# Performance work log

Hardware: AMD Instinct MI355X
Metric: run time of the kernel (lower is better)

## Reference

```python
import jax, jax.numpy as jnp
import numpy as np

LN_EPS = 1e-5

def layer_norm(h, gamma, beta):
    mu = jnp.mean(h, axis=-1, keepdims=True)
    var = jnp.mean(jnp.square(h - mu), axis=-1, keepdims=True)
    return (h - mu) * jax.lax.rsqrt(var + LN_EPS) * gamma + beta

def gcn_conv(x, src, dst, W, b, n_nodes):
    # PyG GCNConv: h = X W; out = D^-1/2 (A + I) D^-1/2 h + b
    h = x @ W
    deg = jax.ops.segment_sum(jnp.ones_like(src, dtype=h.dtype), dst, num_segments=n_nodes)
    dinv = jax.lax.rsqrt(jnp.maximum(deg, 1.0))  # deg >= 1 due to self-loops
    norm = dinv[src] * dinv[dst]                  # [E]
    msg = h[src] * norm[:, None]                  # [E, d]
    return jax.ops.segment_sum(msg, dst, num_segments=n_nodes) + b

def setup_inputs() -> dict:
    key = jax.random.key(0)
    ks = jax.random.split(key, 8)
    N, E, Cin, Ch, Cout = 10000, 160000, 256, 512, 256
    x = jax.random.normal(ks[0], (N, Cin), dtype=jnp.float32)
    edge_index = jax.random.randint(ks[1], (2, E), 0, N, dtype=jnp.int64)
    W1 = jax.random.normal(ks[2], (Cin, Ch), dtype=jnp.float32) * (1.0 / np.sqrt(Cin))
    b1 = jnp.zeros((Ch,), dtype=jnp.float32)
    gamma1 = jnp.ones((Ch,), dtype=jnp.float32)
    beta1 = jnp.zeros((Ch,), dtype=jnp.float32)
    W2 = jax.random.normal(ks[3], (Ch, Cout), dtype=jnp.float32) * (1.0 / np.sqrt(Ch))
    b2 = jnp.zeros((Cout,), dtype=jnp.float32)
    gamma2 = jnp.ones((Cout,), dtype=jnp.float32)
    beta2 = jnp.zeros((Cout,), dtype=jnp.float32)
    return {"x": x, "edge_index": edge_index, "W1": W1, "b1": b1,
            "gamma1": gamma1, "beta1": beta1, "W2": W2, "b2": b2,
            "gamma2": gamma2, "beta2": beta2}

def reference(x, edge_index, W1, b1, gamma1, beta1, W2, b2, gamma2, beta2):
    n = x.shape[0]
    loops = jnp.arange(n, dtype=edge_index.dtype)
    src = jnp.concatenate([edge_index[0], loops])
    dst = jnp.concatenate([edge_index[1], loops])
    h = gcn_conv(x, src, dst, W1, b1, n)
    h = jax.nn.relu(layer_norm(h, gamma1, beta1))  # dropout = identity (eval mode)
    g = gcn_conv(h, src, dst, W2, b2, n)
    g = jax.nn.relu(layer_norm(g, gamma2, beta2))
    return g
```

## Files before the change

### kernel.cpp

```cpp
#include <hip/hip_runtime.h>
#include <hip/hip_bf16.h>


typedef __attribute__((ext_vector_type(8))) short bf16x8;
typedef __attribute__((ext_vector_type(4))) float f32x4;
typedef __attribute__((ext_vector_type(4))) unsigned short us4;
typedef __attribute__((ext_vector_type(8))) unsigned short us8;

__device__ __forceinline__ unsigned short f2bf(float f) {
  unsigned int x = __float_as_uint(f);
  return (unsigned short)((x + 0x7FFFu + ((x >> 16) & 1u)) >> 16);
}
__device__ __forceinline__ float bf2f(unsigned short u) {
  return __uint_as_float((unsigned int)u << 16);
}

__device__ __forceinline__ void transpose_tile(const float* __restrict__ W,
                                               unsigned short* __restrict__ Wt,
                                               int K, int N, int n0, int k0,
                                               unsigned short (*t)[33], int tid) {
  int tx = tid & 31, ty = tid >> 5;
#pragma unroll
  for (int i = 0; i < 32; i += 8)
    t[ty + i][tx] = f2bf(W[(size_t)(k0 + ty + i) * N + n0 + tx]);
  __syncthreads();
#pragma unroll
  for (int i = 0; i < 32; i += 8)
    Wt[(size_t)(n0 + ty + i) * K + k0 + tx] = t[tx][ty + i];
  __syncthreads();
}

__global__ __launch_bounds__(256) void prep_kernel(
    const float* __restrict__ x, unsigned short* __restrict__ xb, long nelem,
    const int* __restrict__ dst, int E, int* __restrict__ deg,
    const float* __restrict__ W1, unsigned short* __restrict__ W1t,
    const float* __restrict__ W2, unsigned short* __restrict__ W2t,
    int Cin, int Ch, int Cout, int nbx, int nbe, int nbw1) {
  __shared__ unsigned short t[32][33];
  int bid = blockIdx.x, tid = threadIdx.x;
  if (bid < nbx) {
    long i = ((long)bid * 256 + tid) * 8;
    if (i + 8 <= nelem) {
      f32x4 a = *(const f32x4*)&x[i];
      f32x4 b = *(const f32x4*)&x[i + 4];
      us8 o;
      o[0] = f2bf(a.x); o[1] = f2bf(a.y); o[2] = f2bf(a.z); o[3] = f2bf(a.w);
      o[4] = f2bf(b.x); o[5] = f2bf(b.y); o[6] = f2bf(b.z); o[7] = f2bf(b.w);
      *(us8*)&xb[i] = o;
    }
  } else if (bid < nbx + nbe) {
    int e = (bid - nbx) * 256 + tid;
    if (e < E) atomicAdd(&deg[dst[e]], 1);
  } else if (bid < nbx + nbe + nbw1) {
    int ti = bid - nbx - nbe;
    int w = Ch >> 5;
    transpose_tile(W1, W1t, Cin, Ch, (ti % w) * 32, (ti / w) * 32, t, tid);
  } else {
    int ti = bid - nbx - nbe - nbw1;
    int w = Cout >> 5;
    transpose_tile(W2, W2t, Ch, Cout, (ti % w) * 32, (ti / w) * 32, t, tid);
  }
}

__global__ __launch_bounds__(1024) void scan_kernel(const int* __restrict__ deg, int N,
                                                    int* __restrict__ offsets,
                                                    int* __restrict__ curs,
                                                    float* __restrict__ dinv) {
  __shared__ int wsum[16];
  __shared__ int chunk_base;
  int tid = threadIdx.x;
  int lane = tid & 63, wid = tid >> 6;
  if (tid == 0) chunk_base = 0;
  __syncthreads();
  for (int c = 0; c < N; c += 1024) {
    int i = c + tid;
    int v = (i < N) ? deg[i] : 0;
    if (i < N) dinv[i] = rsqrtf((float)(v + 1));
    int s = v;
#pragma unroll
    for (int off = 1; off < 64; off <<= 1) {
      int t = __shfl_up(s, off, 64);
      if (lane >= off) s += t;
    }
    if (lane == 63) wsum[wid] = s;
    __syncthreads();
    if (wid == 0 && lane < 16) {
      int ws = wsum[lane];
      int t = ws;
#pragma unroll
      for (int off = 1; off < 16; off <<= 1) {
        int u = __shfl_up(t, off, 64);
        if (lane >= off) t += u;
      }
      wsum[lane] = t - ws;
    }
    __syncthreads();
    if (i < N) {
      int o = chunk_base + wsum[wid] + s - v;
      offsets[i] = o;
      curs[i] = o;
    }
    __syncthreads();
    if (tid == 1023) chunk_base += wsum[15] + s;
  }
  __syncthreads();
  if (tid == 0) offsets[N] = chunk_base;
}

__global__ __launch_bounds__(256) void fill_kernel(const int* __restrict__ src,
                                                   const int* __restrict__ dst, int E,
                                                   int* __restrict__ curs,
                                                   const float* __restrict__ dinv,
                                                   int2* __restrict__ csr_sn) {
  int e = blockIdx.x * 256 + threadIdx.x;
  if (e >= E) return;
  int s = src[e], d = dst[e];
  int p = atomicAdd(&curs[d], 1);
  csr_sn[p] = make_int2(s, __float_as_int(dinv[s] * dinv[d]));
}


#define AGG_FMA(hv, wt)                      \
  acc.x = fmaf(bf2f((hv).x), (wt), acc.x);   \
  acc.y = fmaf(bf2f((hv).y), (wt), acc.y);   \
  acc.z = fmaf(bf2f((hv).z), (wt), acc.z);   \
  acc.w = fmaf(bf2f((hv).w), (wt), acc.w);

template <bool FUSE_LN, typename OutT>
__device__ __forceinline__ void agg_node(int node, int lane,
                                         const unsigned short* __restrict__ H,
                                         const int2* __restrict__ csr,
                                         const int* __restrict__ offs,
                                         const float* __restrict__ dinv,
                                         const float* __restrict__ bias,
                                         const float* __restrict__ gamma,
                                         const float* __restrict__ beta,
                                         OutT* __restrict__ out) {
  int p0 = offs[node], p1 = offs[node + 1];
  int n = p1 - p0;
  f32x4 acc = {0.f, 0.f, 0.f, 0.f};
  if (n > 0) {
    int2 e0 = csr[p0];
    us4 h0 = *(const us4*)&H[(size_t)e0.x * 256 + lane * 4];
    if (n > 1) {
      int2 e1 = csr[p0 + 1];
      for (int p = p0; p + 2 < p1; ++p) {
        us4 h1v = *(const us4*)&H[(size_t)e1.x * 256 + lane * 4];
        int2 e2 = csr[p + 2];
        AGG_FMA(h0, __int_as_float(e0.y));
        e0 = e1; h0 = h1v; e1 = e2;
      }
      us4 h1v = *(const us4*)&H[(size_t)e1.x * 256 + lane * 4];
      AGG_FMA(h0, __int_as_float(e0.y));
      AGG_FMA(h1v, __int_as_float(e1.y));
    } else {
      AGG_FMA(h0, __int_as_float(e0.y));
    }
  }
  float dn = dinv[node];
  us4 sv = *(const us4*)&H[(size_t)node * 256 + lane * 4];
  AGG_FMA(sv, dn * dn);
  if (bias) acc += *(const f32x4*)&bias[lane * 4];
  if constexpr (FUSE_LN) {
    float s  = acc.x + acc.y + acc.z + acc.w;
    float ss = acc.x * acc.x + acc.y * acc.y + acc.z * acc.z + acc.w * acc.w;
#pragma unroll
    for (int off = 32; off > 0; off >>= 1) {
      s  += __shfl_xor(s, off, 64);
      ss += __shfl_xor(ss, off, 64);
    }
    float mu = s * (1.0f / 256.0f);
    float var = ss * (1.0f / 256.0f) - mu * mu;
    float r = rsqrtf(var + 1e-5f);
    f32x4 g  = *(const f32x4*)&gamma[lane * 4];
    f32x4 be = *(const f32x4*)&beta[lane * 4];
    f32x4 o;
    o.x = fmaxf((acc.x - mu) * r * g.x + be.x, 0.f);
    o.y = fmaxf((acc.y - mu) * r * g.y + be.y, 0.f);
    o.z = fmaxf((acc.z - mu) * r * g.z + be.z, 0.f);
    o.w = fmaxf((acc.w - mu) * r * g.w + be.w, 0.f);
    *(f32x4*)&out[(size_t)node * 256 + lane * 4] = o;
  } else {
    us4 o;
    o.x = f2bf(acc.x); o.y = f2bf(acc.y); o.z = f2bf(acc.z); o.w = f2bf(acc.w);
    *(us4*)&out[(size_t)node * 256 + lane * 4] = o;
  }
}

template <bool FUSE_LN, typename OutT>
__global__ __launch_bounds__(256) void agg_kernel(const unsigned short* __restrict__ H,
                                                  const int2* __restrict__ csr,
                                                  const int* __restrict__ offs,
                                                  const float* __restrict__ dinv,
                                                  const float* __restrict__ bias,
                                                  const float* __restrict__ gamma,
                                                  const float* __restrict__ beta,
                                                  OutT* __restrict__ out, int N) {
  int node = blockIdx.x * 4 + (threadIdx.x >> 6);
  if (node >= N) return;
  agg_node<FUSE_LN, OutT>(node, threadIdx.x & 63, H, csr, offs, dinv, bias, gamma, beta, out);
}


template <typename OutT>
__global__ __launch_bounds__(256) void mfma_gemm_kernel(
    const unsigned short* __restrict__ A, const unsigned short* __restrict__ Bt,
    const float* __restrict__ bias, OutT* __restrict__ C, int M, int K, int N) {
  __shared__ unsigned short As[2][64 * 32];
  __shared__ unsigned short Bs[2][128 * 32];
  int tid = threadIdx.x;
  int lane = tid & 63, wid = tid >> 6;
  int bm = blockIdx.x * 64, bn = blockIdx.y * 128;
  int wm = (wid >> 1) * 32, wn = (wid & 1) * 64;
  int srow = tid >> 2;
  int schunk = tid & 3;
  int frow = lane & 15, fk = lane >> 4;
  f32x4 acc[2][4] = {};

  int scA = schunk ^ ((srow >> 1) & 3);
  int gaA = bm + srow; gaA = gaA < M ? gaA : M - 1;
  const unsigned short* gA0 = A + (size_t)gaA * K + scA * 8;
  int rowB0 = srow, rowB1 = 64 + srow;
  int scB0 = schunk ^ ((rowB0 >> 1) & 3);
  int scB1 = schunk ^ ((rowB1 >> 1) & 3);
  const unsigned short* gB0 = Bt + (size_t)(bn + rowB0) * K + scB0 * 8;
  const unsigned short* gB1 = Bt + (size_t)(bn + rowB1) * K + scB1 * 8;

  auto stage = [&](int k0, unsigned short* Ad, unsigned short* Bd) {
    __builtin_amdgcn_global_load_lds(
        (const __attribute__((address_space(1))) unsigned int*)(const void*)(gA0 + k0),
        (__attribute__((address_space(3))) unsigned int*)(void*)(Ad + (wid * 16) * 32),
        16, 0, 0);
    __builtin_amdgcn_global_load_lds(
        (const __attribute__((address_space(1))) unsigned int*)(const void*)(gB0 + k0),
        (__attribute__((address_space(3))) unsigned int*)(void*)(Bd + (wid * 16) * 32),
        16, 0, 0);
    __builtin_amdgcn_global_load_lds(
        (const __attribute__((address_space(1))) unsigned int*)(const void*)(gB1 + k0),
        (__attribute__((address_space(3))) unsigned int*)(void*)(Bd + (64 + wid * 16) * 32),
        16, 0, 0);
  };

  int nk = K >> 5;
  stage(0, As[0], Bs[0]);
  __syncthreads();
  for (int k = 0; k < nk; ++k) {
    unsigned short* Ac = As[k & 1];
    unsigned short* Bc = Bs[k & 1];
    if (k + 1 < nk) stage((k + 1) << 5, As[(k + 1) & 1], Bs[(k + 1) & 1]);
    bf16x8 af[2], bf[4];
#pragma unroll
    for (int mi = 0; mi < 2; ++mi) {
      int row = wm + mi * 16 + frow;
      int sc = fk ^ ((row >> 1) & 3);
      af[mi] = *(const bf16x8*)(Ac + row * 32 + sc * 8);
    }
#pragma unroll
    for (int ni = 0; ni < 4; ++ni) {
      int row = wn + ni * 16 + frow;
      int sc = fk ^ ((row >> 1) & 3);
      bf[ni] = *(const bf16x8*)(Bc + row * 32 + sc * 8);
    }
#pragma unroll
    for (int mi = 0; mi < 2; ++mi)
#pragma unroll
      for (int ni = 0; ni < 4; ++ni)
        acc[mi][ni] = __builtin_amdgcn_mfma_f32_16x16x32_bf16(af[mi], bf[ni], acc[mi][ni], 0, 0, 0);
    __syncthreads();
  }

  int row0 = bm + wm + fk * 4;
  int col0 = bn + wn + frow;
#pragma unroll
  for (int mi = 0; mi < 2; ++mi) {
#pragma unroll
    for (int ni = 0; ni < 4; ++ni) {
      int col = col0 + ni * 16;
      float bv = bias ? bias[col] : 0.0f;
#pragma unroll
      for (int r = 0; r < 4; ++r) {
        int row = row0 + mi * 16 + r;
        if (row < M) {
          float v = acc[mi][ni][r] + bv;
          if constexpr (sizeof(OutT) == 4) C[(size_t)row * N + col] = v;
          else                             C[(size_t)row * N + col] = f2bf(v);
        }
      }
    }
  }
}


__global__ __launch_bounds__(256) void ln_relu512_kernel(const float* __restrict__ in,
                                                         const float* __restrict__ gamma,
                                                         const float* __restrict__ beta,
                                                         unsigned short* __restrict__ out) {
  int row = blockIdx.x;
  const float* p = in + (size_t)row * 512;
  int tid = threadIdx.x;
  float v0 = p[tid];
  float v1 = p[tid + 256];
  float s = v0 + v1;
  float ss = v0 * v0 + v1 * v1;
#pragma unroll
  for (int off = 32; off > 0; off >>= 1) {
    s  += __shfl_down(s, off, 64);
    ss += __shfl_down(ss, off, 64);
  }
  __shared__ float sh[8];
  int wid = tid >> 6;
  if ((tid & 63) == 0) { sh[wid] = s; sh[4 + wid] = ss; }
  __syncthreads();
  s  = sh[0] + sh[1] + sh[2] + sh[3];
  ss = sh[4] + sh[5] + sh[6] + sh[7];
  float mu = s * (1.0f / 512.0f);
  float var = ss * (1.0f / 512.0f) - mu * mu;
  float r = rsqrtf(var + 1e-5f);
  out[(size_t)row * 512 + tid]       = f2bf(fmaxf((v0 - mu) * r * gamma[tid] + beta[tid], 0.0f));
  out[(size_t)row * 512 + tid + 256] = f2bf(fmaxf((v1 - mu) * r * gamma[tid + 256] + beta[tid + 256], 0.0f));
}


extern "C" void kernel_launch(void* const* d_in, const int* in_sizes, int n_in,
                              void* d_out, int out_size, void* d_ws, size_t ws_size,
                              hipStream_t stream) {
  const float* x    = (const float*)d_in[0];
  const int*   ei   = (const int*)d_in[1];
  const float* W1   = (const float*)d_in[2];
  const float* b1   = (const float*)d_in[3];
  const float* ga1  = (const float*)d_in[4];
  const float* be1  = (const float*)d_in[5];
  const float* W2   = (const float*)d_in[6];
  const float* b2   = (const float*)d_in[7];
  const float* ga2  = (const float*)d_in[8];
  const float* be2  = (const float*)d_in[9];
  float* out = (float*)d_out;

  const int Ch   = in_sizes[3];
  const int Cout = in_sizes[7];
  const int Cin  = in_sizes[2] / Ch;
  const int N    = in_sizes[0] / Cin;
  const int E    = in_sizes[1] / 2;
  const int* srcp = ei;
  const int* dstp = ei + E;

  char* ws = (char*)d_ws;
  size_t off = 0;
  auto alloc = [&](size_t bytes) -> void* {
    off = (off + 255) & ~(size_t)255;
    void* p = ws + off;
    off += bytes;
    return p;
  };
  unsigned short* xb   = (unsigned short*)alloc((size_t)N * Cin * 2);
  unsigned short* axb  = (unsigned short*)alloc((size_t)N * Cin * 2);
  float*          h1   = (float*)alloc((size_t)N * Ch * 4);
  unsigned short* h1b  = (unsigned short*)alloc((size_t)N * Ch * 2);
  unsigned short* h2b  = (unsigned short*)alloc((size_t)N * Cout * 2);
  unsigned short* W1t  = (unsigned short*)alloc((size_t)Cin * Ch * 2);
  unsigned short* W2t  = (unsigned short*)alloc((size_t)Ch * Cout * 2);
  int*   deg   = (int*)alloc((size_t)N * 4);
  int*   curs  = (int*)alloc((size_t)N * 4);
  int*   offs  = (int*)alloc((size_t)(N + 1) * 4);
  float* dinv  = (float*)alloc((size_t)N * 4);
  int2*  csr   = (int2*)alloc((size_t)E * 8);

  hipMemsetAsync(deg, 0, (size_t)N * 4, stream);

  long nelem = (long)N * Cin;
  int nbx  = (int)((nelem / 8 + 255) / 256);
  int nbe  = (E + 255) / 256;
  int nbw1 = (Cin / 32) * (Ch / 32);
  int nbw2 = (Ch / 32) * (Cout / 32);
  prep_kernel<<<nbx + nbe + nbw1 + nbw2, 256, 0, stream>>>(
      x, xb, nelem, dstp, E, deg, W1, W1t, W2, W2t, Cin, Ch, Cout, nbx, nbe, nbw1);
  scan_kernel<<<1, 1024, 0, stream>>>(deg, N, offs, curs, dinv);
  fill_kernel<<<nbe, 256, 0, stream>>>(srcp, dstp, E, curs, dinv, csr);

  agg_kernel<false, unsigned short><<<(N + 3) / 4, 256, 0, stream>>>(
      xb, csr, offs, dinv, nullptr, nullptr, nullptr, axb, N);
  mfma_gemm_kernel<float><<<dim3((N + 63) / 64, Ch / 128), 256, 0, stream>>>(
      axb, W1t, b1, h1, N, Cin, Ch);
  ln_relu512_kernel<<<N, 256, 0, stream>>>(h1, ga1, be1, h1b);

  mfma_gemm_kernel<unsigned short><<<dim3((N + 63) / 64, Cout / 128), 256, 0, stream>>>(
      h1b, W2t, nullptr, h2b, N, Ch, Cout);
  agg_kernel<true, float><<<(N + 3) / 4, 256, 0, stream>>>(
      h2b, csr, offs, dinv, b2, ga2, be2, out, N);
}
```

Measured before the change: 189.9 us.

## Reorder layer-1 GCN to GEMM-then-aggregate and fuse LayerNorm into aggregation

Layer 1 now multiplies X by W1 first, then aggregates the 512-wide bf16 result with bias, LayerNorm and ReLU fused into the aggregation kernel. The aggregation kernel is generalised over channel width. This removes the fp32 intermediate and the standalone LayerNorm kernel. In exchange, the sparse gather in layer 1 reads rows twice as wide, and the GEMM output is rounded to bf16 before aggregation.

```diff
diff --git a/kernel.cpp b/kernel.cpp
--- a/kernel.cpp
+++ b/kernel.cpp
@@ -6,6 +6,10 @@
 typedef __attribute__((ext_vector_type(4))) float f32x4;
 typedef __attribute__((ext_vector_type(4))) unsigned short us4;
 typedef __attribute__((ext_vector_type(8))) unsigned short us8;
+
+template <int CW> struct VecT;
+template <> struct VecT<4> { typedef us4 T; };
+template <> struct VecT<8> { typedef us8 T; };
 
 __device__ __forceinline__ unsigned short f2bf(float f) {
   unsigned int x = __float_as_uint(f);
@@ -120,92 +124,77 @@
 }
 
 
-#define AGG_FMA(hv, wt)                      \
-  acc.x = fmaf(bf2f((hv).x), (wt), acc.x);   \
-  acc.y = fmaf(bf2f((hv).y), (wt), acc.y);   \
-  acc.z = fmaf(bf2f((hv).z), (wt), acc.z);   \
-  acc.w = fmaf(bf2f((hv).w), (wt), acc.w);
-
-template <bool FUSE_LN, typename OutT>
-__device__ __forceinline__ void agg_node(int node, int lane,
-                                         const unsigned short* __restrict__ H,
-                                         const int2* __restrict__ csr,
-                                         const int* __restrict__ offs,
-                                         const float* __restrict__ dinv,
-                                         const float* __restrict__ bias,
-                                         const float* __restrict__ gamma,
-                                         const float* __restrict__ beta,
-                                         OutT* __restrict__ out) {
+template <int C, typename OutT>
+__global__ __launch_bounds__(256) void agg_ln_kernel(
+    const unsigned short* __restrict__ H, const int2* __restrict__ csr,
+    const int* __restrict__ offs, const float* __restrict__ dinv,
+    const float* __restrict__ bias, const float* __restrict__ gamma,
+    const float* __restrict__ beta, OutT* __restrict__ out, int N) {
+  constexpr int CW = C / 64;
+  typedef typename VecT<CW>::T usv;
+  int node = blockIdx.x * 4 + (threadIdx.x >> 6);
+  if (node >= N) return;
+  int lane = threadIdx.x & 63;
   int p0 = offs[node], p1 = offs[node + 1];
   int n = p1 - p0;
-  f32x4 acc = {0.f, 0.f, 0.f, 0.f};
+  float acc[CW] = {};
+  auto fma_row = [&](usv hv, float wt) {
+#pragma unroll
+    for (int j = 0; j < CW; ++j) acc[j] = fmaf(bf2f(hv[j]), wt, acc[j]);
+  };
   if (n > 0) {
     int2 e0 = csr[p0];
-    us4 h0 = *(const us4*)&H[(size_t)e0.x * 256 + lane * 4];
+    usv h0 = *(const usv*)&H[(size_t)e0.x * C + lane * CW];
     if (n > 1) {
       int2 e1 = csr[p0 + 1];
       for (int p = p0; p + 2 < p1; ++p) {
-        us4 h1v = *(const us4*)&H[(size_t)e1.x * 256 + lane * 4];
+        usv h1v = *(const usv*)&H[(size_t)e1.x * C + lane * CW];
         int2 e2 = csr[p + 2];
-        AGG_FMA(h0, __int_as_float(e0.y));
+        fma_row(h0, __int_as_float(e0.y));
         e0 = e1; h0 = h1v; e1 = e2;
       }
-      us4 h1v = *(const us4*)&H[(size_t)e1.x * 256 + lane * 4];
-      AGG_FMA(h0, __int_as_float(e0.y));
-      AGG_FMA(h1v, __int_as_float(e1.y));
+      usv h1v = *(const usv*)&H[(size_t)e1.x * C + lane * CW];
+      fma_row(h0, __int_as_float(e0.y));
+      fma_row(h1v, __int_as_float(e1.y));
     } else {
-      AGG_FMA(h0, __int_as_float(e0.y));
+      fma_row(h0, __int_as_float(e0.y));
     }
   }
   float dn = dinv[node];
-  us4 sv = *(const us4*)&H[(size_t)node * 256 + lane * 4];
-  AGG_FMA(sv, dn * dn);
-  if (bias) acc += *(const f32x4*)&bias[lane * 4];
-  if constexpr (FUSE_LN) {
-    float s  = acc.x + acc.y + acc.z + acc.w;
-    float ss = acc.x * acc.x + acc.y * acc.y + acc.z * acc.z + acc.w * acc.w;
-#pragma unroll
-    for (int off = 32; off > 0; off >>= 1) {
-      s  += __shfl_xor(s, off, 64);
-      ss += __shfl_xor(ss, off, 64);
-    }
-    float mu = s * (1.0f / 256.0f);
-    float var = ss * (1.0f / 256.0f) - mu * mu;
-    float r = rsqrtf(var + 1e-5f);
-    f32x4 g  = *(const f32x4*)&gamma[lane * 4];
-    f32x4 be = *(const f32x4*)&beta[lane * 4];
-    f32x4 o;
-    o.x = fmaxf((acc.x - mu) * r * g.x + be.x, 0.f);
-    o.y = fmaxf((acc.y - mu) * r * g.y + be.y, 0.f);
-    o.z = fmaxf((acc.z - mu) * r * g.z + be.z, 0.f);
-    o.w = fmaxf((acc.w - mu) * r * g.w + be.w, 0.f);
-    *(f32x4*)&out[(size_t)node * 256 + lane * 4] = o;
+  usv sv = *(const usv*)&H[(size_t)node * C + lane * CW];
+  fma_row(sv, dn * dn);
+#pragma unroll
+  for (int j = 0; j < CW; ++j) acc[j] += bias[lane * CW + j];
+  float s = 0.f, ss = 0.f;
+#pragma unroll
+  for (int j = 0; j < CW; ++j) { s += acc[j]; ss += acc[j] * acc[j]; }
+#pragma unroll
+  for (int off = 32; off > 0; off >>= 1) {
+    s  += __shfl_xor(s, off, 64);
+    ss += __shfl_xor(ss, off, 64);
+  }
+  float mu = s * (1.0f / C);
+  float var = ss * (1.0f / C) - mu * mu;
+  float r = rsqrtf(var + 1e-5f);
+  float o[CW];
+#pragma unroll
+  for (int j = 0; j < CW; ++j)
+    o[j] = fmaxf((acc[j] - mu) * r * gamma[lane * CW + j] + beta[lane * CW + j], 0.f);
+  if constexpr (sizeof(OutT) == 4) {
+#pragma unroll
+    for (int j = 0; j < CW; ++j) out[(size_t)node * C + lane * CW + j] = o[j];
   } else {
-    us4 o;
-    o.x = f2bf(acc.x); o.y = f2bf(acc.y); o.z = f2bf(acc.z); o.w = f2bf(acc.w);
-    *(us4*)&out[(size_t)node * 256 + lane * 4] = o;
-  }
-}
-
-template <bool FUSE_LN, typename OutT>
-__global__ __launch_bounds__(256) void agg_kernel(const unsigned short* __restrict__ H,
-                                                  const int2* __restrict__ csr,
-                                                  const int* __restrict__ offs,
-                                                  const float* __restrict__ dinv,
-                                                  const float* __restrict__ bias,
-                                                  const float* __restrict__ gamma,
-                                                  const float* __restrict__ beta,
-                                                  OutT* __restrict__ out, int N) {
-  int node = blockIdx.x * 4 + (threadIdx.x >> 6);
-  if (node >= N) return;
-  agg_node<FUSE_LN, OutT>(node, threadIdx.x & 63, H, csr, offs, dinv, bias, gamma, beta, out);
-}
-
-
-template <typename OutT>
+    usv ov;
+#pragma unroll
+    for (int j = 0; j < CW; ++j) ov[j] = f2bf(o[j]);
+    *(usv*)&out[(size_t)node * C + lane * CW] = ov;
+  }
+}
+
+
 __global__ __launch_bounds__(256) void mfma_gemm_kernel(
     const unsigned short* __restrict__ A, const unsigned short* __restrict__ Bt,
-    const float* __restrict__ bias, OutT* __restrict__ C, int M, int K, int N) {
+    unsigned short* __restrict__ C, int M, int K, int N) {
   __shared__ unsigned short As[2][64 * 32];
   __shared__ unsigned short Bs[2][128 * 32];
   int tid = threadIdx.x;
@@ -276,48 +265,13 @@
 #pragma unroll
     for (int ni = 0; ni < 4; ++ni) {
       int col = col0 + ni * 16;
-      float bv = bias ? bias[col] : 0.0f;
 #pragma unroll
       for (int r = 0; r < 4; ++r) {
         int row = row0 + mi * 16 + r;
-        if (row < M) {
-          float v = acc[mi][ni][r] + bv;
-          if constexpr (sizeof(OutT) == 4) C[(size_t)row * N + col] = v;
-          else                             C[(size_t)row * N + col] = f2bf(v);
-        }
+        if (row < M) C[(size_t)row * N + col] = f2bf(acc[mi][ni][r]);
       }
     }
   }
-}
-
-
-__global__ __launch_bounds__(256) void ln_relu512_kernel(const float* __restrict__ in,
-                                                         const float* __restrict__ gamma,
-                                                         const float* __restrict__ beta,
-                                                         unsigned short* __restrict__ out) {
-  int row = blockIdx.x;
-  const float* p = in + (size_t)row * 512;
-  int tid = threadIdx.x;
-  float v0 = p[tid];
-  float v1 = p[tid + 256];
-  float s = v0 + v1;
-  float ss = v0 * v0 + v1 * v1;
-#pragma unroll
-  for (int off = 32; off > 0; off >>= 1) {
-    s  += __shfl_down(s, off, 64);
-    ss += __shfl_down(ss, off, 64);
-  }
-  __shared__ float sh[8];
-  int wid = tid >> 6;
-  if ((tid & 63) == 0) { sh[wid] = s; sh[4 + wid] = ss; }
-  __syncthreads();
-  s  = sh[0] + sh[1] + sh[2] + sh[3];
-  ss = sh[4] + sh[5] + sh[6] + sh[7];
-  float mu = s * (1.0f / 512.0f);
-  float var = ss * (1.0f / 512.0f) - mu * mu;
-  float r = rsqrtf(var + 1e-5f);
-  out[(size_t)row * 512 + tid]       = f2bf(fmaxf((v0 - mu) * r * gamma[tid] + beta[tid], 0.0f));
-  out[(size_t)row * 512 + tid + 256] = f2bf(fmaxf((v1 - mu) * r * gamma[tid + 256] + beta[tid + 256], 0.0f));
 }
 
 
@@ -353,10 +307,9 @@
     return p;
   };
   unsigned short* xb   = (unsigned short*)alloc((size_t)N * Cin * 2);
-  unsigned short* axb  = (unsigned short*)alloc((size_t)N * Cin * 2);
-  float*          h1   = (float*)alloc((size_t)N * Ch * 4);
+  unsigned short* h1w  = (unsigned short*)alloc((size_t)N * Ch * 2);
   unsigned short* h1b  = (unsigned short*)alloc((size_t)N * Ch * 2);
-  unsigned short* h2b  = (unsigned short*)alloc((size_t)N * Cout * 2);
+  unsigned short* h2w  = (unsigned short*)alloc((size_t)N * Cout * 2);
   unsigned short* W1t  = (unsigned short*)alloc((size_t)Cin * Ch * 2);
   unsigned short* W2t  = (unsigned short*)alloc((size_t)Ch * Cout * 2);
   int*   deg   = (int*)alloc((size_t)N * 4);
@@ -377,14 +330,13 @@
   scan_kernel<<<1, 1024, 0, stream>>>(deg, N, offs, curs, dinv);
   fill_kernel<<<nbe, 256, 0, stream>>>(srcp, dstp, E, curs, dinv, csr);
 
-  agg_kernel<false, unsigned short><<<(N + 3) / 4, 256, 0, stream>>>(
-      xb, csr, offs, dinv, nullptr, nullptr, nullptr, axb, N);
-  mfma_gemm_kernel<float><<<dim3((N + 63) / 64, Ch / 128), 256, 0, stream>>>(
-      axb, W1t, b1, h1, N, Cin, Ch);
-  ln_relu512_kernel<<<N, 256, 0, stream>>>(h1, ga1, be1, h1b);
-
-  mfma_gemm_kernel<unsigned short><<<dim3((N + 63) / 64, Cout / 128), 256, 0, stream>>>(
-      h1b, W2t, nullptr, h2b, N, Ch, Cout);
-  agg_kernel<true, float><<<(N + 3) / 4, 256, 0, stream>>>(
-      h2b, csr, offs, dinv, b2, ga2, be2, out, N);
-}
+  mfma_gemm_kernel<<<dim3((N + 63) / 64, Ch / 128), 256, 0, stream>>>(
+      xb, W1t, h1w, N, Cin, Ch);
+  agg_ln_kernel<512, unsigned short><<<(N + 3) / 4, 256, 0, stream>>>(
+      h1w, csr, offs, dinv, b1, ga1, be1, h1b, N);
+
+  mfma_gemm_kernel<<<dim3((N + 63) / 64, Cout / 128), 256, 0, stream>>>(
+      h1b, W2t, h2w, N, Ch, Cout);
+  agg_ln_kernel<256, float><<<(N + 3) / 4, 256, 0, stream>>>(
+      h2w, csr, offs, dinv, b2, ga2, be2, out, N);
+}
```

New measurement: 182.1 us. -4.1%, faster.
